# Optimization experiments

Hardware: AMD Instinct MI355X
Metric: run time of the kernel (lower is better)

## Reference

```python
import jax, jax.numpy as jnp
import numpy as np
import math

B, S, D, E, H = 8, 384, 768, 768, 12
HD = E // H
MAXL = 512

def _xavier(key, shape):
    fan_in, fan_out = shape[1], shape[0]
    lim = math.sqrt(6.0 / (fan_in + fan_out))
    return jax.random.uniform(key, shape, jnp.float32, -lim, lim)

def setup_inputs() -> dict:
    key = jax.random.key(0)
    ks = jax.random.split(key, 12)
    return {
        "x": jax.random.normal(ks[0], (B, S, D), jnp.float32),
        "mask": jnp.ones((B, S), jnp.int32),
        "segment_ids": jax.random.randint(ks[1], (B, S), 0, 2).astype(jnp.int32),
        "sep_distances": jax.random.normal(ks[2], (B, S), jnp.float32),
        "Wq": _xavier(ks[3], (E, D)), "bq": jnp.zeros((E,), jnp.float32),
        "Wk": _xavier(ks[4], (E, D)), "bk": jnp.zeros((E,), jnp.float32),
        "Wv": _xavier(ks[5], (E, D)), "bv": jnp.zeros((E,), jnp.float32),
        "rel_emb": jax.random.normal(ks[6], (2 * MAXL - 1, D), jnp.float32),
        "Wpk": _xavier(ks[7], (E, D)), "bpk": jnp.zeros((E,), jnp.float32),
        "Wpq": _xavier(ks[8], (E, D)), "bpq": jnp.zeros((E,), jnp.float32),
        "same_bias": jnp.zeros((H,), jnp.float32),
        "cross_bias": jnp.zeros((H,), jnp.float32),
        "sep_scale": jnp.full((H,), 0.25, jnp.float32),
        "sep_decay": jnp.full((H,), 0.35, jnp.float32),
        "Wo": _xavier(ks[9], (D, E)), "bo": jnp.zeros((D,), jnp.float32),
    }

def reference(x, mask, segment_ids, sep_distances, Wq, bq, Wk, bk, Wv, bv,
              rel_emb, Wpk, bpk, Wpq, bpq, same_bias, cross_bias,
              sep_scale, sep_decay, Wo, bo):
    b, s, _ = x.shape
    def shape_heads(t):  # [b,s,E] -> [b,H,s,HD]
        return t.reshape(b, s, H, HD).transpose(0, 2, 1, 3)
    q = shape_heads(x @ Wq.T + bq)
    k = shape_heads(x @ Wk.T + bk)
    v = shape_heads(x @ Wv.T + bv)
    # relative positions i - j, clamped and shifted
    rel_pos = jnp.arange(s)[:, None] - jnp.arange(s)[None, :]
    rel_pos = jnp.clip(rel_pos, -(MAXL - 1), MAXL - 1) + (MAXL - 1)
    rel = rel_emb[rel_pos]                     # [s,s,D]
    pos_k = (rel @ Wpk.T + bpk).reshape(s, s, H, HD)  # [i,j,h,d]
    pos_q = (rel @ Wpq.T + bpq).reshape(s, s, H, HD)
    c2c = jnp.einsum('bhid,bhjd->bhij', q, k)
    c2p = jnp.einsum('bhid,ijhd->bhij', q, pos_k)
    p2c = jnp.einsum('ijhd,bhjd->bhij', pos_q, k)
    logits = (c2c + c2p + p2c) / math.sqrt(HD * 3.0)
    # segment bias
    same = (segment_ids[:, :, None] == segment_ids[:, None, :]).astype(jnp.float32)[:, None]  # [b,1,s,s]
    cross = 1.0 - same
    hb = lambda p: p[None, :, None, None]
    seg_bias = same * hb(same_bias) + cross * hb(cross_bias)
    abs_sep = jnp.abs(sep_distances)
    gap = jnp.abs(abs_sep[:, :, None] - abs_sep[:, None, :])[:, None]  # [b,1,s,s]
    decay = jax.nn.softplus(sep_decay)[None, :, None, None] + 1e-4
    seg_bias = seg_bias + cross * jnp.exp(-gap * decay) * hb(sep_scale)
    logits = logits + seg_bias
    # mask: [b,s] -> [b,1,1,s]
    m = mask[:, None, None, :]
    logits = jnp.where(m == 0, jnp.float32(-9e15), logits)
    attn = jax.nn.softmax(logits, axis=-1)
    vals = jnp.einsum('bhij,bhjd->bhid', attn, v)
    vals = vals.transpose(0, 2, 1, 3).reshape(b, s, E)
    return vals @ Wo.T + bo
```

## Files before the change

### kernel.cpp

```cpp
#include <hip/hip_runtime.h>
#include <math.h>

#define B_  8
#define S_  384
#define H_  12
#define HD_ 64
#define E_  768
#define D_  768

typedef float  floatx4 __attribute__((ext_vector_type(4)));
typedef __bf16 bf16x8  __attribute__((ext_vector_type(8)));
typedef unsigned int ux4 __attribute__((ext_vector_type(4)));

__device__ __forceinline__ unsigned short f2bf(float f) {
    union { float f; unsigned u; } x; x.f = f;
    unsigned r = x.u + 0x7fff + ((x.u >> 16) & 1);
    return (unsigned short)(r >> 16);
}
__device__ __forceinline__ float bf2f(unsigned short u) {
    union { unsigned u; float f; } x; x.u = ((unsigned)u) << 16;
    return x.f;
}
__device__ __forceinline__ bf16x8 gld8(const unsigned short* p) {
    return __builtin_bit_cast(bf16x8, *(const ux4*)p);
}
__device__ __forceinline__ int tadr(int row, int cD) {
    return (row * 8 + (cD ^ (row & 7))) * 8;
}
__device__ __forceinline__ bf16x8 lds8(const unsigned short* base, int row, int cD) {
    return __builtin_bit_cast(bf16x8, *(const ux4*)(base + tadr(row, cD)));
}

__global__ __launch_bounds__(256) void convert_all(
    const float* __restrict__ x,
    const float* __restrict__ Wq, const float* __restrict__ Wk,
    const float* __restrict__ Wv, const float* __restrict__ Wo,
    const float* __restrict__ Wpk, const float* __restrict__ Wpq,
    const float* __restrict__ rel128,
    unsigned short* __restrict__ xb,
    unsigned short* __restrict__ wqb, unsigned short* __restrict__ wkb,
    unsigned short* __restrict__ wvb, unsigned short* __restrict__ wob,
    unsigned short* __restrict__ wpkb, unsigned short* __restrict__ wpqb,
    unsigned short* __restrict__ relb)
{
    const int seg = blockIdx.y;
    const int e = (blockIdx.x * 256 + threadIdx.x) * 4;
    const float* src;
    unsigned short* dst;
    if (seg < 4)       { src = x + (size_t)seg * 589824; dst = xb + (size_t)seg * 589824; }
    else if (seg == 4) { src = Wq;  dst = wqb; }
    else if (seg == 5) { src = Wk;  dst = wkb; }
    else if (seg == 6) { src = Wv;  dst = wvb; }
    else if (seg == 7) { src = Wo;  dst = wob; }
    else if (seg == 8) { src = Wpk; dst = wpkb; }
    else if (seg == 9) { src = Wpq; dst = wpqb; }
    else               { src = rel128; dst = relb; }

    float4 v;
    if (seg == 10 && e >= 767 * 768) v = make_float4(0.f, 0.f, 0.f, 0.f);
    else                             v = *(const float4*)(src + e);
    ushort4 o;
    o.x = f2bf(v.x); o.y = f2bf(v.y); o.z = f2bf(v.z); o.w = f2bf(v.w);
    *(ushort4*)(dst + e) = o;
}

__global__ __launch_bounds__(256) void proj_all(
    const unsigned short* __restrict__ xb, const unsigned short* __restrict__ relb,
    const unsigned short* __restrict__ wq, const unsigned short* __restrict__ wk,
    const unsigned short* __restrict__ wv, const unsigned short* __restrict__ wpk,
    const unsigned short* __restrict__ wpq,
    const float* __restrict__ bq, const float* __restrict__ bk,
    const float* __restrict__ bv, const float* __restrict__ bpk,
    const float* __restrict__ bpq,
    unsigned short* __restrict__ qb, unsigned short* __restrict__ kb,
    unsigned short* __restrict__ vtb, unsigned short* __restrict__ pkb,
    unsigned short* __restrict__ pqb)
{
    const int bid = blockIdx.x;
    int z, mt, nt;
    if (bid < 864) {
        z = bid / 288; const int r = bid - z * 288; mt = r / 6; nt = r - mt * 6;
    } else {
        const int r2 = bid - 864; z = 3 + r2 / 72;
        const int r = r2 % 72; mt = r / 6; nt = r - mt * 6;
    }
    const int m0 = mt * 64, n0 = nt * 128;

    const unsigned short* A = (z < 3) ? xb : relb;
    const unsigned short* W = (z == 0) ? wq : (z == 1) ? wk : (z == 2) ? wv
                            : (z == 3) ? wpk : wpq;
    const float* bias = (z == 0) ? bq : (z == 1) ? bk : (z == 2) ? bv
                      : (z == 3) ? bpk : bpq;
    unsigned short* C = (z == 0) ? qb : (z == 1) ? kb : (z == 2) ? vtb
                      : (z == 3) ? pkb : pqb;

    __shared__ unsigned short As[64 * 64];
    __shared__ unsigned short Ws[128 * 64];

    const int tid  = threadIdx.x;
    const int lane = tid & 63;
    const int wv_  = tid >> 6;
    const int quad = lane >> 4, l16 = lane & 15;

    floatx4 acc[4][2];
#pragma unroll
    for (int i = 0; i < 4; ++i)
#pragma unroll
        for (int j = 0; j < 2; ++j) acc[i][j] = (floatx4){0.f, 0.f, 0.f, 0.f};

    for (int k0 = 0; k0 < 768; k0 += 64) {
        __syncthreads();
#pragma unroll
        for (int r = 0; r < 2; ++r) {
            const int idx = tid + 256 * r;
            const int row = idx >> 3, cL = idx & 7, cD = cL ^ (row & 7);
            __builtin_amdgcn_global_load_lds(
                (__attribute__((address_space(1))) void*)(A + (size_t)(m0 + row) * 768 + k0 + cD * 8),
                (__attribute__((address_space(3))) void*)&As[idx * 8], 16, 0, 0);
        }
#pragma unroll
        for (int r = 0; r < 4; ++r) {
            const int idx = tid + 256 * r;
            const int row = idx >> 3, cL = idx & 7, cD = cL ^ (row & 7);
            __builtin_amdgcn_global_load_lds(
                (__attribute__((address_space(1))) void*)(W + (size_t)(n0 + row) * 768 + k0 + cD * 8),
                (__attribute__((address_space(3))) void*)&Ws[idx * 8], 16, 0, 0);
        }
        __syncthreads();

        bf16x8 a[4][2], b[2][2];
#pragma unroll
        for (int mi = 0; mi < 4; ++mi)
#pragma unroll
            for (int kc = 0; kc < 2; ++kc)
                a[mi][kc] = lds8(As, mi * 16 + l16, kc * 4 + quad);
#pragma unroll
        for (int ni = 0; ni < 2; ++ni)
#pragma unroll
            for (int kc = 0; kc < 2; ++kc)
                b[ni][kc] = lds8(Ws, wv_ * 32 + ni * 16 + l16, kc * 4 + quad);
#pragma unroll
        for (int mi = 0; mi < 4; ++mi)
#pragma unroll
            for (int ni = 0; ni < 2; ++ni)
#pragma unroll
                for (int kc = 0; kc < 2; ++kc)
                    acc[mi][ni] = __builtin_amdgcn_mfma_f32_16x16x32_bf16(
                        a[mi][kc], b[ni][kc], acc[mi][ni], 0, 0, 0);
    }

#pragma unroll
    for (int ni = 0; ni < 2; ++ni) {
        const int n = n0 + wv_ * 32 + ni * 16 + l16;
        const float bn = bias[n];
#pragma unroll
        for (int mi = 0; mi < 4; ++mi) {
            const int mbase = m0 + mi * 16 + quad * 4;
            if (z == 2) {
                const int bb = mbase / S_, s = mbase - bb * S_;
                const int h = n >> 6, hd = n & 63;
                ushort4 o;
                o.x = f2bf(acc[mi][ni][0] + bn);
                o.y = f2bf(acc[mi][ni][1] + bn);
                o.z = f2bf(acc[mi][ni][2] + bn);
                o.w = f2bf(acc[mi][ni][3] + bn);
                *(ushort4*)&C[(((size_t)(bb * H_ + h) << 6) + hd) * S_ + s] = o;
            } else if (z < 2) {
#pragma unroll
                for (int reg = 0; reg < 4; ++reg) {
                    const int m = mbase + reg;
                    const int bb = m / S_, s = m - bb * S_;
                    const int h = n >> 6, hd = n & 63;
                    C[(((size_t)(bb * H_ + h) * S_ + s) << 6) + hd] =
                        f2bf(acc[mi][ni][reg] + bn);
                }
            } else {
#pragma unroll
                for (int reg = 0; reg < 4; ++reg)
                    C[(size_t)(mbase + reg) * 768 + n] = f2bf(acc[mi][ni][reg] + bn);
            }
        }
    }
}

__global__ __launch_bounds__(256) void gemm_out(
    const unsigned short* __restrict__ A, const unsigned short* __restrict__ W,
    const float* __restrict__ bias, float* __restrict__ C)
{
    const int mt = blockIdx.x / 6, nt = blockIdx.x - mt * 6;
    const int m0 = mt * 64, n0 = nt * 128;

    __shared__ unsigned short As[64 * 64];
    __shared__ unsigned short Ws[128 * 64];

    const int tid  = threadIdx.x;
    const int lane = tid & 63;
    const int wv_  = tid >> 6;
    const int quad = lane >> 4, l16 = lane & 15;

    floatx4 acc[4][2];
#pragma unroll
    for (int i = 0; i < 4; ++i)
#pragma unroll
        for (int j = 0; j < 2; ++j) acc[i][j] = (floatx4){0.f, 0.f, 0.f, 0.f};

    for (int k0 = 0; k0 < 768; k0 += 64) {
        __syncthreads();
#pragma unroll
        for (int r = 0; r < 2; ++r) {
            const int idx = tid + 256 * r;
            const int row = idx >> 3, cL = idx & 7, cD = cL ^ (row & 7);
            __builtin_amdgcn_global_load_lds(
                (__attribute__((address_space(1))) void*)(A + (size_t)(m0 + row) * 768 + k0 + cD * 8),
                (__attribute__((address_space(3))) void*)&As[idx * 8], 16, 0, 0);
        }
#pragma unroll
        for (int r = 0; r < 4; ++r) {
            const int idx = tid + 256 * r;
            const int row = idx >> 3, cL = idx & 7, cD = cL ^ (row & 7);
            __builtin_amdgcn_global_load_lds(
                (__attribute__((address_space(1))) void*)(W + (size_t)(n0 + row) * 768 + k0 + cD * 8),
                (__attribute__((address_space(3))) void*)&Ws[idx * 8], 16, 0, 0);
        }
        __syncthreads();

        bf16x8 a[4][2], b[2][2];
#pragma unroll
        for (int mi = 0; mi < 4; ++mi)
#pragma unroll
            for (int kc = 0; kc < 2; ++kc)
                a[mi][kc] = lds8(As, mi * 16 + l16, kc * 4 + quad);
#pragma unroll
        for (int ni = 0; ni < 2; ++ni)
#pragma unroll
            for (int kc = 0; kc < 2; ++kc)
                b[ni][kc] = lds8(Ws, wv_ * 32 + ni * 16 + l16, kc * 4 + quad);
#pragma unroll
        for (int mi = 0; mi < 4; ++mi)
#pragma unroll
            for (int ni = 0; ni < 2; ++ni)
#pragma unroll
                for (int kc = 0; kc < 2; ++kc)
                    acc[mi][ni] = __builtin_amdgcn_mfma_f32_16x16x32_bf16(
                        a[mi][kc], b[ni][kc], acc[mi][ni], 0, 0, 0);
    }

#pragma unroll
    for (int ni = 0; ni < 2; ++ni) {
        const int n = n0 + wv_ * 32 + ni * 16 + l16;
        const float bn = bias[n];
#pragma unroll
        for (int mi = 0; mi < 4; ++mi)
#pragma unroll
            for (int reg = 0; reg < 4; ++reg) {
                const int m = m0 + mi * 16 + quad * 4 + reg;
                C[(size_t)m * 768 + n] = acc[mi][ni][reg] + bn;
            }
    }
}

__global__ __launch_bounds__(256, 3) void attn_mfma(
    const unsigned short* __restrict__ qg, const unsigned short* __restrict__ kg,
    const unsigned short* __restrict__ vtg,
    const unsigned short* __restrict__ pkg, const unsigned short* __restrict__ pqg,
    const int* __restrict__ seg, const float* __restrict__ sep,
    const int* __restrict__ mask,
    const float* __restrict__ same_bias, const float* __restrict__ cross_bias,
    const float* __restrict__ sep_scale, const float* __restrict__ sep_decay,
    unsigned short* __restrict__ part_O, float* __restrict__ part_ml)
{
    __shared__ float CP[64 * 68];

    const int tid  = threadIdx.x;
    const int lane = tid & 63, w = tid >> 6;
    const int l16  = lane & 15, quad = lane >> 4;
    const int it = blockIdx.x, h = blockIdx.y;
    const int b  = blockIdx.z / 6, jt = blockIdx.z - 6 * b;
    const int i0 = it * 64, j0 = jt * 64;
    const size_t bh = (size_t)(b * H_ + h);

    const unsigned short* kbase  = kg  + bh * S_ * 64;
    const unsigned short* vtbase = vtg + bh * 64 * S_;
    const int dbase = i0 - j0 + 320;

    bf16x8 qf[2];
#pragma unroll
    for (int ks = 0; ks < 2; ++ks)
        qf[ks] = gld8(qg + (bh * S_ + i0 + 16 * w + l16) * 64 + ks * 32 + quad * 8);

    bf16x8 kf[4][2];
#pragma unroll
    for (int nj = 0; nj < 4; ++nj)
#pragma unroll
        for (int ks = 0; ks < 2; ++ks)
            kf[nj][ks] = gld8(kbase + (size_t)(j0 + 16 * nj + l16) * 64
                              + ks * 32 + quad * 8);

    const int row = 16 * w + l16;
    const float aii = fabsf(sep[b * S_ + i0 + row]);
    const int   sii = seg[b * S_ + i0 + row];
    const float* sepj = sep  + b * S_ + j0;
    const int*   segj = seg  + b * S_ + j0;
    const int*   mskj = mask + b * S_ + j0;
    float ajv[16]; int sjv[16], mkv[16];
    *(float4*)&ajv[0]  = *(const float4*)&sepj[quad * 8];
    *(float4*)&ajv[4]  = *(const float4*)&sepj[quad * 8 + 4];
    *(float4*)&ajv[8]  = *(const float4*)&sepj[32 + quad * 8];
    *(float4*)&ajv[12] = *(const float4*)&sepj[32 + quad * 8 + 4];
    *(int4*)&sjv[0]  = *(const int4*)&segj[quad * 8];
    *(int4*)&sjv[4]  = *(const int4*)&segj[quad * 8 + 4];
    *(int4*)&sjv[8]  = *(const int4*)&segj[32 + quad * 8];
    *(int4*)&sjv[12] = *(const int4*)&segj[32 + quad * 8 + 4];
    *(int4*)&mkv[0]  = *(const int4*)&mskj[quad * 8];
    *(int4*)&mkv[4]  = *(const int4*)&mskj[quad * 8 + 4];
    *(int4*)&mkv[8]  = *(const int4*)&mskj[32 + quad * 8];
    *(int4*)&mkv[12] = *(const int4*)&mskj[32 + quad * 8 + 4];

    const float sb  = same_bias[h];
    const float cb  = cross_bias[h];
    const float ssc = sep_scale[h];
    const float sd  = sep_decay[h];
    const float dec = fmaxf(sd, 0.f) + log1pf(__expf(-fabsf(sd))) + 1e-4f;
    const float isc = 0.07216878364870323f;

#pragma unroll
    for (int nj = 0; nj < 4; ++nj) {
        floatx4 acc = (floatx4){0.f, 0.f, 0.f, 0.f};
#pragma unroll
        for (int ks = 0; ks < 2; ++ks)
            acc = __builtin_amdgcn_mfma_f32_16x16x32_bf16(qf[ks], kf[nj][ks], acc, 0, 0, 0);
#pragma unroll
        for (int reg = 0; reg < 4; ++reg) {
            const int ii = 16 * w + quad * 4 + reg;
            CP[ii * 68 + 16 * nj + l16] = acc[reg];
        }
    }

#pragma unroll
    for (int f = 0; f < 5; ++f) {
        const int nd = w + f;
        floatx4 acc = (floatx4){0.f, 0.f, 0.f, 0.f};
#pragma unroll
        for (int ks = 0; ks < 2; ++ks) {
            bf16x8 bf = gld8(pkg + (size_t)(dbase + 16 * nd + l16) * 768
                             + h * 64 + ks * 32 + quad * 8);
            acc = __builtin_amdgcn_mfma_f32_16x16x32_bf16(qf[ks], bf, acc, 0, 0, 0);
        }
        const int ddloc = 16 * nd + l16;
#pragma unroll
        for (int reg = 0; reg < 4; ++reg) {
            const int ii = 16 * w + quad * 4 + reg;
            const int jj = ii - ddloc + 63;
            if (jj >= 0 && jj < 64)
                CP[ii * 68 + jj] += acc[reg];
        }
    }

#pragma unroll
    for (int f = 0; f < 5; ++f) {
        const int nd = w + f;
        bf16x8 pqf[2];
#pragma unroll
        for (int ks = 0; ks < 2; ++ks)
            pqf[ks] = gld8(pqg + (size_t)(dbase + 16 * nd + l16) * 768
                           + h * 64 + ks * 32 + quad * 8);
#pragma unroll
        for (int g = 0; g < 2; ++g) {
            const int nj = (g == 0) ? (3 - f) : (4 - f);
            if (nj < 0 || nj > 3) continue;
            floatx4 acc = (floatx4){0.f, 0.f, 0.f, 0.f};
#pragma unroll
            for (int ks = 0; ks < 2; ++ks)
                acc = __builtin_amdgcn_mfma_f32_16x16x32_bf16(pqf[ks], kf[nj][ks], acc, 0, 0, 0);
            const int jj = 16 * nj + l16;
#pragma unroll
            for (int reg = 0; reg < 4; ++reg) {
                const int ddloc = 16 * nd + quad * 4 + reg;
                const int ii = ddloc + jj - 63;
                if (ii >= 16 * w && ii < 16 * w + 16)
                    CP[ii * 68 + jj] += acc[reg];
            }
        }
    }

    floatx4 cp0 = *(const floatx4*)&CP[row * 68 + quad * 8];
    floatx4 cp1 = *(const floatx4*)&CP[row * 68 + quad * 8 + 4];
    floatx4 cp2 = *(const floatx4*)&CP[row * 68 + 32 + quad * 8];
    floatx4 cp3 = *(const floatx4*)&CP[row * 68 + 32 + quad * 8 + 4];

    float lg[16];
    float tmax = -INFINITY;
#pragma unroll
    for (int e = 0; e < 16; ++e) {
        const float cpv = (e < 4) ? cp0[e] : (e < 8) ? cp1[e - 4]
                        : (e < 12) ? cp2[e - 8] : cp3[e - 12];
        float xv = cpv * isc;
        const float gap = fabsf(aii - fabsf(ajv[e]));
        const float bias = (sii == sjv[e]) ? sb
                         : cb + __expf(-gap * dec) * ssc;
        xv += bias;
        if (mkv[e] == 0) xv = -9.0e15f;
        lg[e] = xv;
        tmax = fmaxf(tmax, xv);
    }
    tmax = fmaxf(tmax, __shfl_xor(tmax, 16));
    tmax = fmaxf(tmax, __shfl_xor(tmax, 32));

    float rs = 0.f;
    unsigned int pk32[8];
#pragma unroll
    for (int e = 0; e < 8; ++e) {
        const float e0 = __expf(lg[2 * e]     - tmax);
        const float e1 = __expf(lg[2 * e + 1] - tmax);
        rs += e0 + e1;
        pk32[e] = (unsigned)f2bf(e0) | ((unsigned)f2bf(e1) << 16);
    }
    rs += __shfl_xor(rs, 16);
    rs += __shfl_xor(rs, 32);

    float* pml = part_ml + (size_t)(jt * 576 + ((b * H_ + h) * 6 + it)) * 128;
    if (quad == 0) {
        pml[row]      = tmax;
        pml[64 + row] = rs;
    }

    bf16x8 pA[2];
    pA[0] = __builtin_bit_cast(bf16x8, (ux4){pk32[0], pk32[1], pk32[2], pk32[3]});
    pA[1] = __builtin_bit_cast(bf16x8, (ux4){pk32[4], pk32[5], pk32[6], pk32[7]});
    floatx4 O[4];
#pragma unroll
    for (int nd = 0; nd < 4; ++nd) {
        O[nd] = (floatx4){0.f, 0.f, 0.f, 0.f};
#pragma unroll
        for (int ks = 0; ks < 2; ++ks) {
            bf16x8 bf = gld8(vtbase + (size_t)(16 * nd + l16) * S_
                             + j0 + ks * 32 + quad * 8);
            O[nd] = __builtin_amdgcn_mfma_f32_16x16x32_bf16(pA[ks], bf, O[nd], 0, 0, 0);
        }
    }

    unsigned short* pO = part_O + (size_t)(jt * 576 + ((b * H_ + h) * 6 + it)) * 4096;
#pragma unroll
    for (int nd = 0; nd < 4; ++nd) {
        const int d = 16 * nd + l16;
#pragma unroll
        for (int reg = 0; reg < 4; ++reg) {
            const int ii = 16 * w + quad * 4 + reg;
            pO[ii * 64 + d] = f2bf(O[nd][reg]);
        }
    }
}

__global__ __launch_bounds__(256) void merge_attn(
    const unsigned short* __restrict__ part_O, const float* __restrict__ part_ml,
    unsigned short* __restrict__ vals)
{
    const int idx = blockIdx.x;
    const int b  = idx / (H_ * 6);
    const int r  = idx - b * H_ * 6;
    const int h  = r / 6, it = r - h * 6;
    const int tid = threadIdx.x;
    const int ii = tid >> 2, c = (tid & 3) * 16;

    float m[6], l[6];
#pragma unroll
    for (int jc = 0; jc < 6; ++jc) {
        const float* pml = part_ml + (size_t)(jc * 576 + idx) * 128;
        m[jc] = pml[ii];
        l[jc] = pml[64 + ii];
    }
    float M = m[0];
#pragma unroll
    for (int jc = 1; jc < 6; ++jc) M = fmaxf(M, m[jc]);
    float wsum = 0.f, wc[6];
#pragma unroll
    for (int jc = 0; jc < 6; ++jc) {
        wc[jc] = __expf(m[jc] - M);
        wsum += wc[jc] * l[jc];
    }
    const float inv = (wsum > 0.f) ? 1.f / wsum : 0.f;

    float o[16];
#pragma unroll
    for (int e = 0; e < 16; ++e) o[e] = 0.f;
#pragma unroll
    for (int jc = 0; jc < 6; ++jc) {
        const unsigned short* pO = part_O + ((size_t)(jc * 576 + idx)) * 4096
                                 + ii * 64 + c;
        ux4 u0 = *(const ux4*)pO;
        ux4 u1 = *(const ux4*)(pO + 8);
        const unsigned short* us0 = (const unsigned short*)&u0;
        const unsigned short* us1 = (const unsigned short*)&u1;
#pragma unroll
        for (int e = 0; e < 8; ++e) {
            o[e]     += wc[jc] * bf2f(us0[e]);
            o[8 + e] += wc[jc] * bf2f(us1[e]);
        }
    }
    ushort4 w0, w1, w2, w3;
#pragma unroll
    for (int e = 0; e < 4; ++e) {
        ((unsigned short*)&w0)[e] = f2bf(o[e] * inv);
        ((unsigned short*)&w1)[e] = f2bf(o[4 + e] * inv);
        ((unsigned short*)&w2)[e] = f2bf(o[8 + e] * inv);
        ((unsigned short*)&w3)[e] = f2bf(o[12 + e] * inv);
    }
    unsigned short* dst = vals + ((size_t)(b * S_ + it * 64 + ii)) * E_ + h * 64 + c;
    *(ushort4*)(dst)      = w0;
    *(ushort4*)(dst + 4)  = w1;
    *(ushort4*)(dst + 8)  = w2;
    *(ushort4*)(dst + 12) = w3;
}

extern "C" void kernel_launch(void* const* d_in, const int* in_sizes, int n_in,
                              void* d_out, int out_size, void* d_ws, size_t ws_size,
                              hipStream_t stream)
{
    const float* x         = (const float*)d_in[0];
    const int*   mask      = (const int*)d_in[1];
    const int*   seg       = (const int*)d_in[2];
    const float* sep       = (const float*)d_in[3];
    const float* Wq        = (const float*)d_in[4];
    const float* bq        = (const float*)d_in[5];
    const float* Wk        = (const float*)d_in[6];
    const float* bk        = (const float*)d_in[7];
    const float* Wv        = (const float*)d_in[8];
    const float* bv        = (const float*)d_in[9];
    const float* rel_emb   = (const float*)d_in[10];
    const float* Wpk       = (const float*)d_in[11];
    const float* bpk       = (const float*)d_in[12];
    const float* Wpq       = (const float*)d_in[13];
    const float* bpq       = (const float*)d_in[14];
    const float* same_bias = (const float*)d_in[15];
    const float* cross_bias= (const float*)d_in[16];
    const float* sep_scale = (const float*)d_in[17];
    const float* sep_decay = (const float*)d_in[18];
    const float* Wo        = (const float*)d_in[19];
    const float* bo        = (const float*)d_in[20];

    const size_t QKVN = (size_t)B_ * S_ * E_;
    const size_t WN   = (size_t)768 * 768;

    unsigned short* xb    = (unsigned short*)d_ws;
    unsigned short* wqb   = xb   + QKVN;
    unsigned short* wkb   = wqb  + WN;
    unsigned short* wvb   = wkb  + WN;
    unsigned short* wob   = wvb  + WN;
    unsigned short* wpkb  = wob  + WN;
    unsigned short* wpqb  = wpkb + WN;
    unsigned short* relb  = wpqb + WN;
    unsigned short* qb    = relb + WN;
    unsigned short* kb    = qb   + QKVN;
    unsigned short* vtb   = kb   + QKVN;
    unsigned short* pkb   = vtb  + QKVN;
    unsigned short* pqb   = pkb  + WN;
    unsigned short* valsb = pqb  + WN;
    unsigned short* partO = valsb + QKVN;
    float*          partml= (float*)(partO + (size_t)6 * 576 * 4096);

    convert_all<<<dim3(576, 11), 256, 0, stream>>>(
        x, Wq, Wk, Wv, Wo, Wpk, Wpq, rel_emb + (size_t)128 * D_,
        xb, wqb, wkb, wvb, wob, wpkb, wpqb, relb);

    proj_all<<<dim3(1008), 256, 0, stream>>>(
        xb, relb, wqb, wkb, wvb, wpkb, wpqb,
        bq, bk, bv, bpk, bpq, qb, kb, vtb, pkb, pqb);

    attn_mfma<<<dim3(6, 12, 48), 256, 0, stream>>>(
        qb, kb, vtb, pkb, pqb, seg, sep, mask,
        same_bias, cross_bias, sep_scale, sep_decay, partO, partml);

    merge_attn<<<dim3(576), 256, 0, stream>>>(partO, partml, valsb);

    gemm_out<<<dim3(288), 256, 0, stream>>>(valsb, wob, bo, (float*)d_out);
}
```

Baseline: 220.3 us.

## Prefetch pos/V fragments up front, hoist bias math, and predicate LDS scatter via trash slot

Issues every global load of the positional-key, positional-query and V^T fragments at kernel start so their latency overlaps the content-to-content MFMA work. The segment/separation bias and the mask bits are computed before the score phase. Branchy LDS adds are replaced by unconditional adds whose invalid lanes write to an extra trash row in shared memory. The large number of live fragments raises register pressure, so the occupancy hint is lowered from 3 to 2 blocks per SM.

```diff
diff --git a/kernel.cpp b/kernel.cpp
--- a/kernel.cpp
+++ b/kernel.cpp
@@ -259,7 +259,7 @@
     }
 }
 
-__global__ __launch_bounds__(256, 3) void attn_mfma(
+__global__ __launch_bounds__(256, 2) void attn_mfma(
     const unsigned short* __restrict__ qg, const unsigned short* __restrict__ kg,
     const unsigned short* __restrict__ vtg,
     const unsigned short* __restrict__ pkg, const unsigned short* __restrict__ pqg,
@@ -269,7 +269,7 @@
     const float* __restrict__ sep_scale, const float* __restrict__ sep_decay,
     unsigned short* __restrict__ part_O, float* __restrict__ part_ml)
 {
-    __shared__ float CP[64 * 68];
+    __shared__ float CP[65 * 68];
 
     const int tid  = threadIdx.x;
     const int lane = tid & 63, w = tid >> 6;
@@ -295,6 +295,25 @@
         for (int ks = 0; ks < 2; ++ks)
             kf[nj][ks] = gld8(kbase + (size_t)(j0 + 16 * nj + l16) * 64
                               + ks * 32 + quad * 8);
+
+    bf16x8 pkf[5][2], pqf[5][2];
+#pragma unroll
+    for (int f = 0; f < 5; ++f)
+#pragma unroll
+        for (int ks = 0; ks < 2; ++ks) {
+            const size_t go = (size_t)(dbase + 16 * (w + f) + l16) * 768
+                            + h * 64 + ks * 32 + quad * 8;
+            pkf[f][ks] = gld8(pkg + go);
+            pqf[f][ks] = gld8(pqg + go);
+        }
+
+    bf16x8 vtf[4][2];
+#pragma unroll
+    for (int nd = 0; nd < 4; ++nd)
+#pragma unroll
+        for (int ks = 0; ks < 2; ++ks)
+            vtf[nd][ks] = gld8(vtbase + (size_t)(16 * nd + l16) * S_
+                               + j0 + ks * 32 + quad * 8);
 
     const int row = 16 * w + l16;
     const float aii = fabsf(sep[b * S_ + i0 + row]);
@@ -323,6 +342,16 @@
     const float dec = fmaxf(sd, 0.f) + log1pf(__expf(-fabsf(sd))) + 1e-4f;
     const float isc = 0.07216878364870323f;
 
+    float biasv[16]; unsigned mkbits = 0;
+#pragma unroll
+    for (int e = 0; e < 16; ++e) {
+        const float gap = fabsf(aii - fabsf(ajv[e]));
+        biasv[e] = (sii == sjv[e]) ? sb : cb + __expf(-gap * dec) * ssc;
+        mkbits |= (mkv[e] != 0 ? 1u : 0u) << e;
+    }
+
+    const int TRASH = 64 * 68;
+
 #pragma unroll
     for (int nj = 0; nj < 4; ++nj) {
         floatx4 acc = (floatx4){0.f, 0.f, 0.f, 0.f};
@@ -338,32 +367,23 @@
 
 #pragma unroll
     for (int f = 0; f < 5; ++f) {
-        const int nd = w + f;
         floatx4 acc = (floatx4){0.f, 0.f, 0.f, 0.f};
 #pragma unroll
-        for (int ks = 0; ks < 2; ++ks) {
-            bf16x8 bf = gld8(pkg + (size_t)(dbase + 16 * nd + l16) * 768
-                             + h * 64 + ks * 32 + quad * 8);
-            acc = __builtin_amdgcn_mfma_f32_16x16x32_bf16(qf[ks], bf, acc, 0, 0, 0);
-        }
-        const int ddloc = 16 * nd + l16;
+        for (int ks = 0; ks < 2; ++ks)
+            acc = __builtin_amdgcn_mfma_f32_16x16x32_bf16(qf[ks], pkf[f][ks], acc, 0, 0, 0);
+        const int ddloc = 16 * (w + f) + l16;
 #pragma unroll
         for (int reg = 0; reg < 4; ++reg) {
             const int ii = 16 * w + quad * 4 + reg;
             const int jj = ii - ddloc + 63;
-            if (jj >= 0 && jj < 64)
-                CP[ii * 68 + jj] += acc[reg];
+            const bool v = (jj >= 0 && jj < 64);
+            const int adr = v ? (ii * 68 + jj) : (TRASH + lane);
+            CP[adr] += acc[reg];
         }
     }
 
 #pragma unroll
     for (int f = 0; f < 5; ++f) {
-        const int nd = w + f;
-        bf16x8 pqf[2];
-#pragma unroll
-        for (int ks = 0; ks < 2; ++ks)
-            pqf[ks] = gld8(pqg + (size_t)(dbase + 16 * nd + l16) * 768
-                           + h * 64 + ks * 32 + quad * 8);
 #pragma unroll
         for (int g = 0; g < 2; ++g) {
             const int nj = (g == 0) ? (3 - f) : (4 - f);
@@ -371,14 +391,15 @@
             floatx4 acc = (floatx4){0.f, 0.f, 0.f, 0.f};
 #pragma unroll
             for (int ks = 0; ks < 2; ++ks)
-                acc = __builtin_amdgcn_mfma_f32_16x16x32_bf16(pqf[ks], kf[nj][ks], acc, 0, 0, 0);
+                acc = __builtin_amdgcn_mfma_f32_16x16x32_bf16(pqf[f][ks], kf[nj][ks], acc, 0, 0, 0);
             const int jj = 16 * nj + l16;
 #pragma unroll
             for (int reg = 0; reg < 4; ++reg) {
-                const int ddloc = 16 * nd + quad * 4 + reg;
+                const int ddloc = 16 * (w + f) + quad * 4 + reg;
                 const int ii = ddloc + jj - 63;
-                if (ii >= 16 * w && ii < 16 * w + 16)
-                    CP[ii * 68 + jj] += acc[reg];
+                const bool v = (ii >= 16 * w && ii < 16 * w + 16);
+                const int adr = v ? (ii * 68 + jj) : (TRASH + lane);
+                CP[adr] += acc[reg];
             }
         }
     }
@@ -394,12 +415,8 @@
     for (int e = 0; e < 16; ++e) {
         const float cpv = (e < 4) ? cp0[e] : (e < 8) ? cp1[e - 4]
                         : (e < 12) ? cp2[e - 8] : cp3[e - 12];
-        float xv = cpv * isc;
-        const float gap = fabsf(aii - fabsf(ajv[e]));
-        const float bias = (sii == sjv[e]) ? sb
-                         : cb + __expf(-gap * dec) * ssc;
-        xv += bias;
-        if (mkv[e] == 0) xv = -9.0e15f;
+        float xv = cpv * isc + biasv[e];
+        if (!((mkbits >> e) & 1u)) xv = -9.0e15f;
         lg[e] = xv;
         tmax = fmaxf(tmax, xv);
     }
@@ -432,11 +449,8 @@
     for (int nd = 0; nd < 4; ++nd) {
         O[nd] = (floatx4){0.f, 0.f, 0.f, 0.f};
 #pragma unroll
-        for (int ks = 0; ks < 2; ++ks) {
-            bf16x8 bf = gld8(vtbase + (size_t)(16 * nd + l16) * S_
-                             + j0 + ks * 32 + quad * 8);
-            O[nd] = __builtin_amdgcn_mfma_f32_16x16x32_bf16(pA[ks], bf, O[nd], 0, 0, 0);
-        }
+        for (int ks = 0; ks < 2; ++ks)
+            O[nd] = __builtin_amdgcn_mfma_f32_16x16x32_bf16(pA[ks], vtf[nd][ks], O[nd], 0, 0, 0);
     }
 
     unsigned short* pO = part_O + (size_t)(jt * 576 + ((b * H_ + h) * 6 + it)) * 4096;
```

Result: no change. 221.5 us (+0.5%).

## Stage positional tiles in LDS via async loads, prefetch V and hoist bias

Applied to the files above, without the earlier changes.

The 128x64 pos_k and pos_q tiles for each block are now loaded with global_load_lds into swizzled shared memory, then read from LDS. Before, each wave fetched overlapping rows of these tiles straight from global memory. V^T fragments are also fetched at kernel start, and the segment/separation bias and mask bits are computed before the MFMA phase so that their latency overlaps the matrix work. In exchange, each block uses about 32 KB more LDS, needs an extra barrier, and holds more live registers (vtf, biasv), which may hurt occupancy under the 3-blocks-per-CU bound.

```diff
diff --git a/kernel.cpp b/kernel.cpp
--- a/kernel.cpp
+++ b/kernel.cpp
@@ -269,6 +269,8 @@
     const float* __restrict__ sep_scale, const float* __restrict__ sep_decay,
     unsigned short* __restrict__ part_O, float* __restrict__ part_ml)
 {
+    __shared__ unsigned short PKs[128 * 64];
+    __shared__ unsigned short PQs[128 * 64];
     __shared__ float CP[64 * 68];
 
     const int tid  = threadIdx.x;
@@ -283,6 +285,19 @@
     const unsigned short* vtbase = vtg + bh * 64 * S_;
     const int dbase = i0 - j0 + 320;
 
+#pragma unroll
+    for (int r = 0; r < 4; ++r) {
+        const int idx = tid + 256 * r;
+        const int srow = idx >> 3, cL = idx & 7, cD = cL ^ (srow & 7);
+        const size_t go = (size_t)(dbase + srow) * 768 + h * 64 + cD * 8;
+        __builtin_amdgcn_global_load_lds(
+            (__attribute__((address_space(1))) void*)(pkg + go),
+            (__attribute__((address_space(3))) void*)&PKs[idx * 8], 16, 0, 0);
+        __builtin_amdgcn_global_load_lds(
+            (__attribute__((address_space(1))) void*)(pqg + go),
+            (__attribute__((address_space(3))) void*)&PQs[idx * 8], 16, 0, 0);
+    }
+
     bf16x8 qf[2];
 #pragma unroll
     for (int ks = 0; ks < 2; ++ks)
@@ -295,6 +310,14 @@
         for (int ks = 0; ks < 2; ++ks)
             kf[nj][ks] = gld8(kbase + (size_t)(j0 + 16 * nj + l16) * 64
                               + ks * 32 + quad * 8);
+
+    bf16x8 vtf[4][2];
+#pragma unroll
+    for (int nd = 0; nd < 4; ++nd)
+#pragma unroll
+        for (int ks = 0; ks < 2; ++ks)
+            vtf[nd][ks] = gld8(vtbase + (size_t)(16 * nd + l16) * S_
+                               + j0 + ks * 32 + quad * 8);
 
     const int row = 16 * w + l16;
     const float aii = fabsf(sep[b * S_ + i0 + row]);
@@ -323,6 +346,14 @@
     const float dec = fmaxf(sd, 0.f) + log1pf(__expf(-fabsf(sd))) + 1e-4f;
     const float isc = 0.07216878364870323f;
 
+    float biasv[16]; unsigned mkbits = 0;
+#pragma unroll
+    for (int e = 0; e < 16; ++e) {
+        const float gap = fabsf(aii - fabsf(ajv[e]));
+        biasv[e] = (sii == sjv[e]) ? sb : cb + __expf(-gap * dec) * ssc;
+        mkbits |= (mkv[e] != 0 ? 1u : 0u) << e;
+    }
+
 #pragma unroll
     for (int nj = 0; nj < 4; ++nj) {
         floatx4 acc = (floatx4){0.f, 0.f, 0.f, 0.f};
@@ -336,14 +367,15 @@
         }
     }
 
+    __syncthreads();
+
 #pragma unroll
     for (int f = 0; f < 5; ++f) {
         const int nd = w + f;
         floatx4 acc = (floatx4){0.f, 0.f, 0.f, 0.f};
 #pragma unroll
         for (int ks = 0; ks < 2; ++ks) {
-            bf16x8 bf = gld8(pkg + (size_t)(dbase + 16 * nd + l16) * 768
-                             + h * 64 + ks * 32 + quad * 8);
+            bf16x8 bf = lds8(PKs, 16 * nd + l16, ks * 4 + quad);
             acc = __builtin_amdgcn_mfma_f32_16x16x32_bf16(qf[ks], bf, acc, 0, 0, 0);
         }
         const int ddloc = 16 * nd + l16;
@@ -362,8 +394,7 @@
         bf16x8 pqf[2];
 #pragma unroll
         for (int ks = 0; ks < 2; ++ks)
-            pqf[ks] = gld8(pqg + (size_t)(dbase + 16 * nd + l16) * 768
-                           + h * 64 + ks * 32 + quad * 8);
+            pqf[ks] = lds8(PQs, 16 * nd + l16, ks * 4 + quad);
 #pragma unroll
         for (int g = 0; g < 2; ++g) {
             const int nj = (g == 0) ? (3 - f) : (4 - f);
@@ -394,12 +425,8 @@
     for (int e = 0; e < 16; ++e) {
         const float cpv = (e < 4) ? cp0[e] : (e < 8) ? cp1[e - 4]
                         : (e < 12) ? cp2[e - 8] : cp3[e - 12];
-        float xv = cpv * isc;
-        const float gap = fabsf(aii - fabsf(ajv[e]));
-        const float bias = (sii == sjv[e]) ? sb
-                         : cb + __expf(-gap * dec) * ssc;
-        xv += bias;
-        if (mkv[e] == 0) xv = -9.0e15f;
+        float xv = cpv * isc + biasv[e];
+        if (!((mkbits >> e) & 1u)) xv = -9.0e15f;
         lg[e] = xv;
         tmax = fmaxf(tmax, xv);
     }
@@ -432,11 +459,8 @@
     for (int nd = 0; nd < 4; ++nd) {
         O[nd] = (floatx4){0.f, 0.f, 0.f, 0.f};
 #pragma unroll
-        for (int ks = 0; ks < 2; ++ks) {
-            bf16x8 bf = gld8(vtbase + (size_t)(16 * nd + l16) * S_
-                             + j0 + ks * 32 + quad * 8);
-            O[nd] = __builtin_amdgcn_mfma_f32_16x16x32_bf16(pA[ks], bf, O[nd], 0, 0, 0);
-        }
+        for (int ks = 0; ks < 2; ++ks)
+            O[nd] = __builtin_amdgcn_mfma_f32_16x16x32_bf16(pA[ks], vtf[nd][ks], O[nd], 0, 0, 0);
     }
 
     unsigned short* pO = part_O + (size_t)(jt * 576 + ((b * H_ + h) * 6 + it)) * 4096;
```

After: 200.9 us, median of 2. 8.8% less time.
